# Kernel tuning notes

Measured on AMD Instinct MI355X. Metric: run time of the kernel, lower is better.

Reference implementation:

```python
import jax, jax.numpy as jnp
import numpy as np

N_FFT = 512
HOP = 128
WIN = 512
Q = 0.1
PCT_WIN = 31
FREQ_WIN = 5
TIME_WIN = 9
STRENGTH = 0.35
THRESH = 1.5
TEMP = 0.15
MIN_MASK = 0.08


def _hann_periodic(n):
    # matches torch.hann_window(n) (periodic)
    return (0.5 * (1.0 - jnp.cos(2.0 * jnp.pi * jnp.arange(n) / n))).astype(jnp.float32)


def _stft(x, window):
    # x: (B, L) -> complex (B, F, T); center=True, reflect pad
    pad = N_FFT // 2
    xp = jnp.pad(x, ((0, 0), (pad, pad)), mode='reflect')
    T = 1 + (xp.shape[-1] - N_FFT) // HOP
    idx = (jnp.arange(T) * HOP)[:, None] + jnp.arange(N_FFT)  # (T, n_fft)
    frames = xp[:, idx] * window  # (B, T, n_fft)
    return jnp.fft.rfft(frames, axis=-1).transpose(0, 2, 1)  # (B, F, T)


def _istft(spec, window, length):
    # spec: (B, F, T) complex -> (B, length)
    frames = jnp.fft.irfft(spec.transpose(0, 2, 1), n=N_FFT, axis=-1) * window  # (B,T,n_fft)
    B, T, _ = frames.shape
    total = N_FFT + HOP * (T - 1)
    idx = ((jnp.arange(T) * HOP)[:, None] + jnp.arange(N_FFT)).ravel()
    out = jnp.zeros((B, total), frames.dtype).at[:, idx].add(frames.reshape(B, -1))
    wsq = jnp.zeros((total,), frames.dtype).at[idx].add(
        jnp.broadcast_to(window ** 2, (T, N_FFT)).ravel())
    out = out / jnp.maximum(wsq, 1e-11)
    pad = N_FFT // 2
    return out[:, pad:pad + length]


def _rolling_quantile(mag):
    # mag: (B, F, T); replicate pad + sliding window of PCT_WIN along time
    p = PCT_WIN // 2
    padded = jnp.pad(mag, ((0, 0), (0, 0), (p, p)), mode='edge')
    T = mag.shape[-1]
    windows = jnp.stack([padded[..., i:i + T] for i in range(PCT_WIN)], axis=-1)  # (B,F,T,W)
    return jnp.quantile(windows, Q, axis=-1)


def _avg_pool(x, k, axis):
    # stride-1 avg pool with zero pad k//2, count_include_pad=True (torch default)
    if k <= 1:
        return x
    p = k // 2
    pads = [(0, 0)] * x.ndim
    pads[axis] = (p, p)
    xp = jnp.pad(x, pads)
    n = x.shape[axis]
    acc = 0.0
    for i in range(k):
        sl = [slice(None)] * x.ndim
        sl[axis] = slice(i, i + n)
        acc = acc + xp[tuple(sl)]
    return acc / k


def setup_inputs() -> dict:
    key = jax.random.key(0)
    k1, k2 = jax.random.split(key)
    B, L = 16, 160000
    noisy = jax.random.normal(k1, (B, L), dtype=jnp.float32)
    enhanced = jax.random.normal(k2, (B, L), dtype=jnp.float32)
    return {"noisy": noisy, "enhanced": enhanced}


def reference(noisy, enhanced):
    length = enhanced.shape[-1]
    window = _hann_periodic(WIN)
    e_spec = _stft(enhanced, window)
    n_spec = _stft(noisy, window)
    e_mag = jnp.maximum(jnp.abs(e_spec), 1e-6)
    n_mag = jnp.maximum(jnp.abs(n_spec), 1e-6)
    # mode == 'sg_input_floor': source is the noisy magnitude
    floor = _rolling_quantile(n_mag)
    floor = _avg_pool(floor, FREQ_WIN, axis=-2)
    floor = _avg_pool(floor, TIME_WIN, axis=-1)
    floor = jnp.maximum(floor, 1e-6)
    mask = jax.nn.sigmoid((e_mag - THRESH * floor) / (TEMP * floor + 1e-6))
    final_mask = MIN_MASK + (1.0 - MIN_MASK) * (1.0 - STRENGTH + STRENGTH * mask)
    phase = e_spec / jnp.maximum(jnp.abs(e_spec), 1e-12)  # unit-phase, = polar(1, angle)
    gated_spec = (e_mag * final_mask).astype(jnp.float32) * phase
    return _istft(gated_spec, window, length)
```

## Files before the change

kernel.cpp:

```cpp
#include <hip/hip_runtime.h>
#include <hip/hip_bf16.h>
#include <math.h>

#define BATCH 16
#define LEN   160000
#define NFFT  512
#define HOP   128
#define NT    1251
#define NF    257
#define PADC  256
#define TWO_PI 6.28318530717958647692f
#define P(i) ((i) + ((i) >> 5))
#define FBUF 528
#define GSTR 264

__device__ __forceinline__ int reflect_idx(int j) {
    j = j < 0 ? -j : j;
    j = j >= LEN ? 2*LEN - 2 - j : j;
    return j;
}

__device__ __forceinline__ float hann(int n) {
    return 0.5f - 0.5f * __cosf(TWO_PI * (float)n * (1.0f / 512.0f));
}

__device__ __forceinline__ __hip_bfloat162 pack_bf2(float x, float y) {
    __hip_bfloat162 r; r.x = __float2bfloat16(x); r.y = __float2bfloat16(y); return r;
}
__device__ __forceinline__ float2 unpack_bf2(__hip_bfloat162 v) {
    return make_float2(__bfloat162float(v.x), __bfloat162float(v.y));
}

struct T4 { float m0, m1, m2, m3; };

__device__ __forceinline__ void ins(T4& a, float v) {
    const float x0 = fminf(a.m0, v);  const float c0 = fmaxf(a.m0, v);
    const float x1 = fminf(a.m1, c0); const float c1 = fmaxf(a.m1, c0);
    const float x2 = fminf(a.m2, c1); const float c2 = fmaxf(a.m2, c1);
    const float x3 = fminf(a.m3, c2);
    a.m0 = x0; a.m1 = x1; a.m2 = x2; a.m3 = x3;
}

__device__ __forceinline__ T4 merge4(const T4& a, const T4& b) {
    const float l0 = fminf(a.m0, b.m3);
    const float l1 = fminf(a.m1, b.m2);
    const float l2 = fminf(a.m2, b.m1);
    const float l3 = fminf(a.m3, b.m0);
    const float t0 = fminf(l0, l2), t2 = fmaxf(l0, l2);
    const float t1 = fminf(l1, l3), t3 = fmaxf(l1, l3);
    T4 r;
    r.m0 = fminf(t0, t1); r.m1 = fmaxf(t0, t1);
    r.m2 = fminf(t2, t3); r.m3 = fmaxf(t2, t3);
    return r;
}

__device__ __forceinline__ T4 sort4(float a, float b, float c, float d) {
    const float x0 = fminf(a, b), x1 = fmaxf(a, b);
    const float x2 = fminf(c, d), x3 = fmaxf(c, d);
    const float y0 = fminf(x0, x2), y2 = fmaxf(x0, x2);
    const float y1 = fminf(x1, x3), y3 = fmaxf(x1, x3);
    T4 r; r.m0 = y0; r.m1 = fminf(y1, y2); r.m2 = fmaxf(y1, y2); r.m3 = y3;
    return r;
}

__device__ __forceinline__ void dft8(float vr[8], float vi[8], float sign) {
    const float K = 0.70710678118654752f;
    float ar=vr[0]+vr[4], ai=vi[0]+vi[4];
    float br=vr[0]-vr[4], bi=vi[0]-vi[4];
    float cr=vr[2]+vr[6], ci=vi[2]+vi[6];
    float dr=vr[2]-vr[6], di=vi[2]-vi[6];
    float er=vr[1]+vr[5], ei=vi[1]+vi[5];
    float fr=vr[1]-vr[5], fi=vi[1]-vi[5];
    float gr=vr[3]+vr[7], gi=vi[3]+vi[7];
    float hr=vr[3]-vr[7], hi=vi[3]-vi[7];
    const float W4dr = -sign*di, W4di = sign*dr;
    const float W4hr = -sign*hi, W4hi = sign*hr;
    const float E0r=ar+cr, E0i=ai+ci, E2r=ar-cr, E2i=ai-ci;
    const float E1r=br+W4dr, E1i=bi+W4di, E3r=br-W4dr, E3i=bi-W4di;
    const float O0r=er+gr, O0i=ei+gi, O2r=er-gr, O2i=ei-gi;
    const float O1r=fr+W4hr, O1i=fi+W4hi, O3r=fr-W4hr, O3i=fi-W4hi;
    const float T1r = K*(O1r - sign*O1i), T1i = K*(O1i + sign*O1r);
    const float T2r = -sign*O2i,          T2i = sign*O2r;
    const float T3r = K*(-O3r - sign*O3i), T3i = K*(-O3i + sign*O3r);
    vr[0]=E0r+O0r; vi[0]=E0i+O0i;  vr[4]=E0r-O0r; vi[4]=E0i-O0i;
    vr[1]=E1r+T1r; vi[1]=E1i+T1i;  vr[5]=E1r-T1r; vi[5]=E1i-T1i;
    vr[2]=E2r+T2r; vi[2]=E2i+T2i;  vr[6]=E2r-T2r; vi[6]=E2i-T2i;
    vr[3]=E3r+T3r; vi[3]=E3i+T3i;  vr[7]=E3r-T3r; vi[7]=E3i-T3i;
}

template<int NS>
__device__ __forceinline__ void fft_pass(float* R, float* I, int j, float sign) {
    float vr[8], vi[8];
    #pragma unroll
    for (int r = 0; r < 8; ++r) { vr[r] = R[P(j + 64*r)]; vi[r] = I[P(j + 64*r)]; }
    const float th = sign * (TWO_PI / (8.0f * (float)NS)) * (float)(j & (NS - 1));
    float w1r, w1i; __sincosf(th, &w1i, &w1r);
    float wr = w1r, wi = w1i;
    #pragma unroll
    for (int r = 1; r < 8; ++r) {
        const float tr = vr[r]*wr - vi[r]*wi;
        vi[r] = vr[r]*wi + vi[r]*wr; vr[r] = tr;
        const float nwr = wr*w1r - wi*w1i;
        wi = wr*w1i + wi*w1r; wr = nwr;
    }
    dft8(vr, vi, sign);
    const int base = ((j / NS) * (8 * NS)) + (j & (NS - 1));
    #pragma unroll
    for (int r = 0; r < 8; ++r) { R[P(base + r*NS)] = vr[r]; I[P(base + r*NS)] = vi[r]; }
}

__device__ __forceinline__ void fft_pass_last(const float* R, const float* I, int j,
                                              float sign, float vr[8], float vi[8]) {
    #pragma unroll
    for (int r = 0; r < 8; ++r) { vr[r] = R[P(j + 64*r)]; vi[r] = I[P(j + 64*r)]; }
    const float th = sign * (TWO_PI / 512.0f) * (float)j;
    float w1r, w1i; __sincosf(th, &w1i, &w1r);
    float wr = w1r, wi = w1i;
    #pragma unroll
    for (int r = 1; r < 8; ++r) {
        const float tr = vr[r]*wr - vi[r]*wi;
        vi[r] = vr[r]*wi + vi[r]*wr; vr[r] = tr;
        const float nwr = wr*w1r - wi*w1i;
        wi = wr*w1i + wi*w1r; wr = nwr;
    }
    dft8(vr, vi, sign);
}

__global__ __launch_bounds__(256, 6) void stft_kernel(const float* __restrict__ enh,
                                                      const float* __restrict__ noi,
                                                      __hip_bfloat162* __restrict__ e_spec,
                                                      __hip_bfloat16*  __restrict__ n_mag) {
    __shared__ float Ar[4*FBUF], Ai[4*FBUF];
    const int tid = threadIdx.x;
    const int w = tid >> 6, j = tid & 63;
    const int tr_ = blockIdx.x * 4 + w;
    const bool live = tr_ < NT;
    const int t = live ? tr_ : NT - 1;
    const int b = blockIdx.y;
    float* ar = Ar + w*FBUF; float* ai = Ai + w*FBUF;

    {
        const int sbase = t * HOP - PADC;
        float vr[8], vi[8];
        if (sbase >= 0 && sbase + NFFT <= LEN) {
            const float* __restrict__ pe = enh + b * LEN + sbase;
            const float* __restrict__ pn = noi + b * LEN + sbase;
            #pragma unroll
            for (int r = 0; r < 8; ++r) {
                const int n = j + 64*r;
                const float wd = hann(n);
                vr[r] = pe[n] * wd;
                vi[r] = pn[n] * wd;
            }
        } else {
            const float* __restrict__ pe = enh + b * LEN;
            const float* __restrict__ pn = noi + b * LEN;
            #pragma unroll
            for (int r = 0; r < 8; ++r) {
                const int n = j + 64*r;
                const int idx = reflect_idx(sbase + n);
                const float wd = hann(n);
                vr[r] = pe[idx] * wd;
                vi[r] = pn[idx] * wd;
            }
        }
        dft8(vr, vi, -1.0f);
        #pragma unroll
        for (int r = 0; r < 8; ++r) { ar[P(8*j + r)] = vr[r]; ai[P(8*j + r)] = vi[r]; }
    }
    fft_pass<8>(ar, ai, j, -1.0f);
    float zr[8], zi[8];
    fft_pass_last(ar, ai, j, -1.0f, zr, zi);

    const int src = (64 - j) & 63;
    float pr[4], pi_[4];
    #pragma unroll
    for (int q = 4; q < 8; ++q) {
        pr[q-4]  = __shfl(zr[q], src);
        pi_[q-4] = __shfl(zi[q], src);
    }
    if (live) {
        const int obase = (b * NT + t) * NF;
        #pragma unroll
        for (int r = 0; r < 4; ++r) {
            const int kk = j + 64*r;
            const float yr = (j == 0) ? zr[(8 - r) & 7] : pr[3 - r];
            const float yi = (j == 0) ? zi[(8 - r) & 7] : pi_[3 - r];
            const float er = 0.5f*(zr[r] + yr), ei = 0.5f*(zi[r] - yi);
            const float nr = 0.5f*(zi[r] + yi), ni = 0.5f*(yr - zr[r]);
            e_spec[obase + kk] = pack_bf2(er, ei);
            n_mag[obase + kk] = __float2bfloat16(fmaxf(sqrtf(nr*nr + ni*ni), 1e-6f));
        }
        if (j == 0) {
            e_spec[obase + 256] = pack_bf2(zr[4], 0.0f);
            n_mag[obase + 256] = __float2bfloat16(fmaxf(fabsf(zi[4]), 1e-6f));
        }
    }
}

__global__ __launch_bounds__(256) void floor_kernel(const __hip_bfloat16* __restrict__ n_mag,
                                                    float* __restrict__ floor_) {
    __shared__ float q[24][GSTR];
    __shared__ float fq[24];
    const int tid = threadIdx.x;
    const int t0 = blockIdx.x * 16, b = blockIdx.y;
    const __hip_bfloat16* __restrict__ pb = n_mag + b * NT * NF;

    {
        float wv[54];
        #pragma unroll
        for (int r = 0; r < 54; ++r) {
            int tr = t0 - 19 + r;
            tr = tr < 0 ? 0 : (tr > NT - 1 ? NT - 1 : tr);
            wv[r] = __bfloat162float(pb[tr * NF + tid]);
        }
        T4 ch[6];
        #pragma unroll
        for (int c = 0; c < 6; ++c)
            ch[c] = merge4(sort4(wv[8*c],   wv[8*c+1], wv[8*c+2], wv[8*c+3]),
                           sort4(wv[8*c+4], wv[8*c+5], wv[8*c+6], wv[8*c+7]));
        #pragma unroll
        for (int k = 0; k < 24; ++k) {
            const int c0 = (k + 7) >> 3;
            T4 m = merge4(merge4(ch[c0], ch[c0+1]), ch[c0+2]);
            #pragma unroll
            for (int jj = k; jj < 8*c0; ++jj) ins(m, wv[jj]);
            #pragma unroll
            for (int jj = 8*c0 + 24; jj < k + 31; ++jj) ins(m, wv[jj]);
            q[k][tid] = m.m3;
        }
    }
    if (tid < 24) {
        const int k = tid;
        T4 m; m.m0 = m.m1 = m.m2 = m.m3 = 3.4e38f;
        for (int dt = -15; dt <= 15; ++dt) {
            int tt = t0 - 4 + k + dt;
            tt = tt < 0 ? 0 : (tt > NT - 1 ? NT - 1 : tt);
            ins(m, __bfloat162float(pb[tt * NF + 256]));
        }
        q[k][256] = m.m3;
    }
    __syncthreads();

    float fp[24];
    {
        const int f = tid;
        #pragma unroll
        for (int k = 0; k < 24; ++k) {
            float acc = 0.0f;
            #pragma unroll
            for (int df = -2; df <= 2; ++df) {
                const int ff = f + df;
                if (ff >= 0 && ff < NF) acc += q[k][ff];
            }
            fp[k] = acc * (1.0f / 5.0f);
        }
    }
    if (tid < 24) {
        const int k = tid;
        fq[k] = (q[k][254] + q[k][255] + q[k][256]) * (1.0f / 5.0f);
    }
    __syncthreads();

    {
        const int f = tid;
        #pragma unroll
        for (int k = 0; k < 24; ++k) {
            const int tq = t0 - 4 + k;
            fp[k] = (tq >= 0 && tq < NT) ? fp[k] : 0.0f;
        }
        float acc = 0.0f;
        #pragma unroll
        for (int k = 0; k < 9; ++k) acc += fp[k];
        #pragma unroll
        for (int to = 0; to < 16; ++to) {
            const int t = t0 + to;
            if (t < NT)
                floor_[(b * NT + t) * NF + f] = fmaxf(acc * (1.0f / 9.0f), 1e-6f);
            if (to < 15) acc += fp[to + 9] - fp[to];
        }
    }
    if (tid < 16) {
        const int to = tid;
        const int t = t0 + to;
        if (t < NT) {
            float acc = 0.0f;
            #pragma unroll
            for (int k = 0; k < 9; ++k) {
                const int tq = t0 - 4 + to + k;
                acc += (tq >= 0 && tq < NT) ? fq[to + k] : 0.0f;
            }
            floor_[(b * NT + t) * NF + 256] = fmaxf(acc * (1.0f / 9.0f), 1e-6f);
        }
    }
}

__global__ __launch_bounds__(256, 6) void istft_ola_kernel(const __hip_bfloat162* __restrict__ g,
                                                           const float* __restrict__ floor_,
                                                           float* __restrict__ out) {
    __shared__ float gr[8*GSTR], gi[8*GSTR];
    const int tid = threadIdx.x;
    const int w = tid >> 6, j = tid & 63;
    const int t0 = blockIdx.x * 8, b = blockIdx.y;
    const int ta = t0 + 2*w;

    float* g0r = gr + (2*w) * GSTR;      float* g0i = gi + (2*w) * GSTR;
    float* g1r = gr + (2*w + 1) * GSTR;  float* g1i = gi + (2*w + 1) * GSTR;

    for (int e = j; e < 2 * NF; e += 64) {
        const int h = (e >= NF) ? 1 : 0;
        const int kk = e - h * NF;
        const int t = ta + h;
        float grv = 0.0f, giv = 0.0f;
        if (t < NT) {
            const int idx = (b * NT + t) * NF + kk;
            const float fl = floor_[idx];
            const float2 e2 = unpack_bf2(g[idx]);
            const float a = sqrtf(e2.x * e2.x + e2.y * e2.y);
            const float emag = fmaxf(a, 1e-6f);
            const float xarg = (emag - 1.5f * fl) / (0.15f * fl + 1e-6f);
            const float mask = 1.0f / (1.0f + __expf(-xarg));
            const float fm = 0.08f + 0.92f * (0.65f + 0.35f * mask);
            const float scale = emag * fm / fmaxf(a, 1e-12f);
            grv = e2.x * scale; giv = e2.y * scale;
        }
        gr[(2*w + h) * GSTR + kk] = grv;
        gi[(2*w + h) * GSTR + kk] = giv;
    }

    float* ar = g0r;
    float* ai = g0i;

    {
        float vr[8], vi[8];
        #pragma unroll
        for (int r = 0; r < 8; ++r) {
            const int n = j + 64*r;
            float cr, ci;
            if (n <= 256) {
                cr = g0r[n] - g1i[n];
                ci = g0i[n] + g1r[n];
            } else {
                const int m = 512 - n;
                cr = g0r[m] + g1i[m];
                ci = g1r[m] - g0i[m];
            }
            vr[r] = cr; vi[r] = ci;
        }
        dft8(vr, vi, 1.0f);
        #pragma unroll
        for (int r = 0; r < 8; ++r) { ar[P(8*j + r)] = vr[r]; ai[P(8*j + r)] = vi[r]; }
    }
    fft_pass<8>(ar, ai, j, 1.0f);
    float xr[8], xi[8];
    fft_pass_last(ar, ai, j, 1.0f, xr, xi);

    #pragma unroll
    for (int r = 0; r < 8; ++r) {
        const int n = j + 64*r;
        const float wd = hann(n) * (1.0f / 512.0f);
        ar[P(n)] = xr[r] * wd;
        ai[P(n)] = xi[r] * wd;
    }
    __syncthreads();

    const int i0 = t0 << 7;
    for (int s = tid; s < 1408; s += 256) {
        const int i = i0 + s;
        const int jj = i - PADC;
        if (jj < 0 || jj >= LEN) continue;
        const int tl = (i >= 384) ? ((i - 384) >> 7) : 0;
        int th = i >> 7; if (th > NT - 1) th = NT - 1;
        const int ca = tl > t0 ? tl : t0;
        const int cb = th < t0 + 7 ? th : t0 + 7;
        if (cb < ca) continue;
        float acc = 0.0f;
        for (int t = ca; t <= cb; ++t) {
            const int ft = t - t0;
            const int n = i - (t << 7);
            acc += ((ft & 1) ? gi : gr)[(ft >> 1) * FBUF + P(n)];
        }
        float winv;
        if (th - tl == 3) winv = (2.0f / 3.0f);
        else {
            float wacc = 0.0f;
            for (int t = tl; t <= th; ++t) {
                const float wd = hann(i - (t << 7));
                wacc += wd * wd;
            }
            winv = 1.0f / fmaxf(wacc, 1e-11f);
        }
        const float v = acc * winv;
        if (tl >= t0 && th <= t0 + 7) out[b * LEN + jj] = v;
        else atomicAdd(out + b * LEN + jj, v);
    }
}

extern "C" void kernel_launch(void* const* d_in, const int* in_sizes, int n_in,
                              void* d_out, int out_size, void* d_ws, size_t ws_size,
                              hipStream_t stream) {
    const float* noisy    = (const float*)d_in[0];
    const float* enhanced = (const float*)d_in[1];
    float* out = (float*)d_out;

    float* ws = (float*)d_ws;
    __hip_bfloat162* e_spec = (__hip_bfloat162*)ws;
    float* floor_ = ws + 5144112;
    __hip_bfloat16* n_mag = (__hip_bfloat16*)(ws + 10288224);

    stft_kernel <<<dim3((NT + 3) / 4, BATCH), dim3(256), 0, stream>>>(enhanced, noisy, e_spec, n_mag);
    floor_kernel<<<dim3((NT + 15) / 16, BATCH), dim3(256), 0, stream>>>(n_mag, floor_);
    hipMemsetAsync(out, 0, (size_t)BATCH * LEN * sizeof(float), stream);
    istft_ola_kernel<<<dim3((NT + 7) / 8, BATCH), dim3(256), 0, stream>>>(e_spec, floor_, out);
}
```

Before: 146.0 us.

## Fuse floor computation into iSTFT kernel and fold output zeroing into STFT

The rolling-quantile noise floor is now computed inside the iSTFT/OLA kernel for each 8-frame tile, so the fp32 floor tensor is never written to or read from global memory. The separate memset of the output is removed; each STFT block zeroes a 512-sample slice of the output instead. This saves one kernel launch, one memset and a large intermediate round trip. In exchange, every fused block recomputes a 46-frame quantile halo for only 8 output frames, which is proportionally more redundant sort work than before, and register pressure is higher.

```diff
diff --git a/kernel.cpp b/kernel.cpp
--- a/kernel.cpp
+++ b/kernel.cpp
@@ -129,7 +129,8 @@
 __global__ __launch_bounds__(256, 6) void stft_kernel(const float* __restrict__ enh,
                                                       const float* __restrict__ noi,
                                                       __hip_bfloat162* __restrict__ e_spec,
-                                                      __hip_bfloat16*  __restrict__ n_mag) {
+                                                      __hip_bfloat16*  __restrict__ n_mag,
+                                                      float* __restrict__ out) {
     __shared__ float Ar[4*FBUF], Ai[4*FBUF];
     const int tid = threadIdx.x;
     const int w = tid >> 6, j = tid & 63;
@@ -140,6 +141,11 @@
     float* ar = Ar + w*FBUF; float* ai = Ai + w*FBUF;
 
     {
+        const int z = (blockIdx.x << 9) + (tid << 1);
+        if (z < LEN) *reinterpret_cast<float2*>(out + (size_t)b * LEN + z) = make_float2(0.0f, 0.0f);
+    }
+
+    {
         const int sbase = t * HOP - PADC;
         float vr[8], vi[8];
         if (sbase >= 0 && sbase + NFFT <= LEN) {
@@ -198,29 +204,36 @@
     }
 }
 
-__global__ __launch_bounds__(256) void floor_kernel(const __hip_bfloat16* __restrict__ n_mag,
-                                                    float* __restrict__ floor_) {
-    __shared__ float q[24][GSTR];
-    __shared__ float fq[24];
+__global__ __launch_bounds__(256, 4) void floor_mask_istft_kernel(
+        const __hip_bfloat162* __restrict__ g,
+        const __hip_bfloat16* __restrict__ n_mag,
+        float* __restrict__ out) {
+    __shared__ float smem[16 * GSTR];
+    __shared__ float fq[16];
+    float (*q)[GSTR] = reinterpret_cast<float (*)[GSTR]>(smem);
+    float* gr = smem;
+    float* gi = smem + 8 * GSTR;
+
     const int tid = threadIdx.x;
-    const int t0 = blockIdx.x * 16, b = blockIdx.y;
+    const int w = tid >> 6, j = tid & 63;
+    const int t0 = blockIdx.x * 8, b = blockIdx.y;
     const __hip_bfloat16* __restrict__ pb = n_mag + b * NT * NF;
 
     {
-        float wv[54];
-        #pragma unroll
-        for (int r = 0; r < 54; ++r) {
+        float wv[46];
+        #pragma unroll
+        for (int r = 0; r < 46; ++r) {
             int tr = t0 - 19 + r;
             tr = tr < 0 ? 0 : (tr > NT - 1 ? NT - 1 : tr);
             wv[r] = __bfloat162float(pb[tr * NF + tid]);
         }
-        T4 ch[6];
-        #pragma unroll
-        for (int c = 0; c < 6; ++c)
+        T4 ch[5];
+        #pragma unroll
+        for (int c = 0; c < 5; ++c)
             ch[c] = merge4(sort4(wv[8*c],   wv[8*c+1], wv[8*c+2], wv[8*c+3]),
                            sort4(wv[8*c+4], wv[8*c+5], wv[8*c+6], wv[8*c+7]));
         #pragma unroll
-        for (int k = 0; k < 24; ++k) {
+        for (int k = 0; k < 16; ++k) {
             const int c0 = (k + 7) >> 3;
             T4 m = merge4(merge4(ch[c0], ch[c0+1]), ch[c0+2]);
             #pragma unroll
@@ -230,7 +243,7 @@
             q[k][tid] = m.m3;
         }
     }
-    if (tid < 24) {
+    if (tid < 16) {
         const int k = tid;
         T4 m; m.m0 = m.m1 = m.m2 = m.m3 = 3.4e38f;
         for (int dt = -15; dt <= 15; ++dt) {
@@ -242,11 +255,11 @@
     }
     __syncthreads();
 
-    float fp[24];
+    float fp[16];
     {
         const int f = tid;
         #pragma unroll
-        for (int k = 0; k < 24; ++k) {
+        for (int k = 0; k < 16; ++k) {
             float acc = 0.0f;
             #pragma unroll
             for (int df = -2; df <= 2; ++df) {
@@ -256,16 +269,13 @@
             fp[k] = acc * (1.0f / 5.0f);
         }
     }
-    if (tid < 24) {
-        const int k = tid;
-        fq[k] = (q[k][254] + q[k][255] + q[k][256]) * (1.0f / 5.0f);
-    }
+    if (tid < 16) fq[tid] = (q[tid][254] + q[tid][255] + q[tid][256]) * (1.0f / 5.0f);
     __syncthreads();
 
-    {
-        const int f = tid;
-        #pragma unroll
-        for (int k = 0; k < 24; ++k) {
+    float flv[8];
+    {
+        #pragma unroll
+        for (int k = 0; k < 16; ++k) {
             const int tq = t0 - 4 + k;
             fp[k] = (tq >= 0 && tq < NT) ? fp[k] : 0.0f;
         }
@@ -273,49 +283,46 @@
         #pragma unroll
         for (int k = 0; k < 9; ++k) acc += fp[k];
         #pragma unroll
-        for (int to = 0; to < 16; ++to) {
-            const int t = t0 + to;
-            if (t < NT)
-                floor_[(b * NT + t) * NF + f] = fmaxf(acc * (1.0f / 9.0f), 1e-6f);
-            if (to < 15) acc += fp[to + 9] - fp[to];
-        }
-    }
-    if (tid < 16) {
-        const int to = tid;
-        const int t = t0 + to;
+        for (int to = 0; to < 8; ++to) {
+            flv[to] = fmaxf(acc * (1.0f / 9.0f), 1e-6f);
+            if (to < 7) acc += fp[to + 9] - fp[to];
+        }
+    }
+
+    {
+        const int f = tid;
+        #pragma unroll
+        for (int ft = 0; ft < 8; ++ft) {
+            const int t = t0 + ft;
+            float grv = 0.0f, giv = 0.0f;
+            if (t < NT) {
+                const float fl = flv[ft];
+                const float2 e2 = unpack_bf2(g[(b * NT + t) * NF + f]);
+                const float a = sqrtf(e2.x * e2.x + e2.y * e2.y);
+                const float emag = fmaxf(a, 1e-6f);
+                const float xarg = (emag - 1.5f * fl) / (0.15f * fl + 1e-6f);
+                const float mask = 1.0f / (1.0f + __expf(-xarg));
+                const float fm = 0.08f + 0.92f * (0.65f + 0.35f * mask);
+                const float scale = emag * fm / fmaxf(a, 1e-12f);
+                grv = e2.x * scale; giv = e2.y * scale;
+            }
+            gr[ft * GSTR + f] = grv;
+            gi[ft * GSTR + f] = giv;
+        }
+    }
+    if (tid < 8) {
+        const int ft = tid;
+        const int t = t0 + ft;
+        float grv = 0.0f, giv = 0.0f;
         if (t < NT) {
             float acc = 0.0f;
             #pragma unroll
             for (int k = 0; k < 9; ++k) {
-                const int tq = t0 - 4 + to + k;
-                acc += (tq >= 0 && tq < NT) ? fq[to + k] : 0.0f;
-            }
-            floor_[(b * NT + t) * NF + 256] = fmaxf(acc * (1.0f / 9.0f), 1e-6f);
-        }
-    }
-}
-
-__global__ __launch_bounds__(256, 6) void istft_ola_kernel(const __hip_bfloat162* __restrict__ g,
-                                                           const float* __restrict__ floor_,
-                                                           float* __restrict__ out) {
-    __shared__ float gr[8*GSTR], gi[8*GSTR];
-    const int tid = threadIdx.x;
-    const int w = tid >> 6, j = tid & 63;
-    const int t0 = blockIdx.x * 8, b = blockIdx.y;
-    const int ta = t0 + 2*w;
-
-    float* g0r = gr + (2*w) * GSTR;      float* g0i = gi + (2*w) * GSTR;
-    float* g1r = gr + (2*w + 1) * GSTR;  float* g1i = gi + (2*w + 1) * GSTR;
-
-    for (int e = j; e < 2 * NF; e += 64) {
-        const int h = (e >= NF) ? 1 : 0;
-        const int kk = e - h * NF;
-        const int t = ta + h;
-        float grv = 0.0f, giv = 0.0f;
-        if (t < NT) {
-            const int idx = (b * NT + t) * NF + kk;
-            const float fl = floor_[idx];
-            const float2 e2 = unpack_bf2(g[idx]);
+                const int tq = t0 - 4 + ft + k;
+                acc += (tq >= 0 && tq < NT) ? fq[ft + k] : 0.0f;
+            }
+            const float fl = fmaxf(acc * (1.0f / 9.0f), 1e-6f);
+            const float2 e2 = unpack_bf2(g[(b * NT + t) * NF + 256]);
             const float a = sqrtf(e2.x * e2.x + e2.y * e2.y);
             const float emag = fmaxf(a, 1e-6f);
             const float xarg = (emag - 1.5f * fl) / (0.15f * fl + 1e-6f);
@@ -324,10 +331,13 @@
             const float scale = emag * fm / fmaxf(a, 1e-12f);
             grv = e2.x * scale; giv = e2.y * scale;
         }
-        gr[(2*w + h) * GSTR + kk] = grv;
-        gi[(2*w + h) * GSTR + kk] = giv;
-    }
-
+        gr[ft * GSTR + 256] = grv;
+        gi[ft * GSTR + 256] = giv;
+    }
+    __syncthreads();
+
+    float* g0r = gr + (2*w) * GSTR;      float* g0i = gi + (2*w) * GSTR;
+    float* g1r = gr + (2*w + 1) * GSTR;  float* g1i = gi + (2*w + 1) * GSTR;
     float* ar = g0r;
     float* ai = g0i;
 
@@ -405,11 +415,8 @@
 
     float* ws = (float*)d_ws;
     __hip_bfloat162* e_spec = (__hip_bfloat162*)ws;
-    float* floor_ = ws + 5144112;
-    __hip_bfloat16* n_mag = (__hip_bfloat16*)(ws + 10288224);
-
-    stft_kernel <<<dim3((NT + 3) / 4, BATCH), dim3(256), 0, stream>>>(enhanced, noisy, e_spec, n_mag);
-    floor_kernel<<<dim3((NT + 15) / 16, BATCH), dim3(256), 0, stream>>>(n_mag, floor_);
-    hipMemsetAsync(out, 0, (size_t)BATCH * LEN * sizeof(float), stream);
-    istft_ola_kernel<<<dim3((NT + 7) / 8, BATCH), dim3(256), 0, stream>>>(e_spec, floor_, out);
-}
+    __hip_bfloat16* n_mag = (__hip_bfloat16*)(ws + 5144112);
+
+    stft_kernel<<<dim3((NT + 3) / 4, BATCH), dim3(256), 0, stream>>>(enhanced, noisy, e_spec, n_mag, out);
+    floor_mask_istft_kernel<<<dim3((NT + 7) / 8, BATCH), dim3(256), 0, stream>>>(e_spec, n_mag, out);
+}
```

Measured after the change: 136.2 us. 6.7% less time.
